# Kernel optimization log

Hardware: AMD Instinct MI355X
Metric: run time of the kernel (lower is better)

Reference implementation:

```python
import jax, jax.numpy as jnp
import numpy as np

B, T, D = 512, 64, 512      # batch, encoder seq len, input_dim
H, A = 256, 256             # hidden_dim, attention_dim (= embed dim)
C = 96                      # num_classes = len(charsets) + 2
STEPS = 26                  # max_len_labels + 1
STD = 0.01


def setup_inputs() -> dict:
    key = jax.random.key(0)
    ks = jax.random.split(key, 14)
    n = lambda k, shape: STD * jax.random.normal(k, shape, jnp.float32)
    return {
        "img": jax.random.normal(ks[0], (B, T, D), jnp.float32),
        "label": jax.random.randint(ks[1], (B, STEPS), 0, C + 1),
        # MLP attention cell
        "Wx": n(ks[2], (A, D)), "bx": jnp.zeros((A,), jnp.float32),
        "Ws": n(ks[3], (A, H)), "bs": jnp.zeros((A,), jnp.float32),
        "Ww": n(ks[4], (1, A)), "bw": jnp.zeros((1,), jnp.float32),
        # target embedding (num_classes + 1 rows)
        "emb": n(ks[5], (C + 1, A)),
        # single-layer GRU, input size D + A, hidden H (torch gate order r,z,n)
        "Wih": n(ks[6], (3 * H, D + A)), "bih": jnp.zeros((3 * H,), jnp.float32),
        "Whh": n(ks[7], (3 * H, H)),     "bhh": jnp.zeros((3 * H,), jnp.float32),
        # output FC
        "Wfc": n(ks[8], (C, H)), "bfc": jnp.zeros((C,), jnp.float32),
    }


def reference(img, label, Wx, bx, Ws, bs, Ww, bw, emb, Wih, Whh, bih, bhh, Wfc, bfc):
    # Precompute xProj once: it is constant across decode steps.
    xProj = jnp.einsum('btd,ad->bta', img, Wx) + bx          # [B,T,A]
    # Teacher forcing: y at step 0 is 0 ([GO]); step i>=1 uses label[:, i].
    y_seq = label.at[:, 0].set(0)                            # [B,STEPS]

    def step(h, y):                                          # h: [B,H], y: [B]
        sProj = h @ Ws.T + bs                                # [B,A]
        e = jnp.tanh(sProj[:, None, :] + xProj)              # [B,T,A]
        v = jnp.einsum('bta,a->bt', e, Ww[0]) + bw[0]        # [B,T]
        alpha = jax.nn.softmax(v, axis=1)
        ctx = jnp.einsum('bt,btd->bd', alpha, img)           # [B,D]
        g = jnp.concatenate([emb[y], ctx], axis=1)           # [B,A+D]
        gi = g @ Wih.T + bih                                 # [B,3H]
        gh = h @ Whh.T + bhh                                 # [B,3H]
        r = jax.nn.sigmoid(gi[:, :H] + gh[:, :H])
        z = jax.nn.sigmoid(gi[:, H:2 * H] + gh[:, H:2 * H])
        nn_ = jnp.tanh(gi[:, 2 * H:] + r * gh[:, 2 * H:])
        h_new = (1.0 - z) * nn_ + z * h
        out = h_new @ Wfc.T + bfc                            # [B,C]
        return h_new, out

    h0 = jnp.zeros((img.shape[0], H), img.dtype)
    _, outs = jax.lax.scan(step, h0, y_seq.T)                # [STEPS,B,C]
    return jnp.transpose(outs, (1, 0, 2))                    # [B,STEPS,C]
```

## Files before the change

kernel.cpp:

```cpp
#include <hip/hip_runtime.h>
#include <math.h>

#define NB 512
#define NT 64
#define ND 512
#define NH 256
#define NA 256
#define NC 96
#define NSTEPS 26
#define NGRU 1152
#define KGRU 768

typedef __attribute__((ext_vector_type(8))) short short8;
typedef __attribute__((ext_vector_type(4))) float f32x4;

static __device__ __forceinline__ unsigned short f2bf(float f) {
    unsigned int u = __float_as_uint(f);
    unsigned int r = (u + 0x7FFFu + ((u >> 16) & 1u)) >> 16;
    return (unsigned short)r;
}
static __device__ __forceinline__ float bf2f(unsigned short u) {
    return __uint_as_float(((unsigned int)u) << 16);
}

__global__ __launch_bounds__(256) void k_prep(
    const float* __restrict__ Wx, const float* __restrict__ Ws,
    const float* __restrict__ Wfc, const float* __restrict__ Wih,
    const float* __restrict__ Whh,
    unsigned short* __restrict__ Wxbf, unsigned short* __restrict__ Wsbf,
    unsigned short* __restrict__ WfcT, unsigned short* __restrict__ Wp)
{
    const int idx = blockIdx.x * 256 + threadIdx.x;
    if (idx < NGRU * KGRU) {
        const int n = idx / KGRU, k = idx - n * KGRU;
        float val = 0.f;
        if (n < 1024) {
            const int j = n >> 2, g = n & 3;
            if (k < 512) {
                if (g == 0)      val = Wih[j * 768 + 256 + k];
                else if (g == 1) val = Wih[(256 + j) * 768 + 256 + k];
                else if (g == 2) val = Wih[(512 + j) * 768 + 256 + k];
            } else {
                const int kh = k - 512;
                if (g == 0)      val = Whh[j * 256 + kh];
                else if (g == 1) val = Whh[(256 + j) * 256 + kh];
                else if (g == 3) val = Whh[(512 + j) * 256 + kh];
            }
        } else if (n < 1120) {
            if (k >= 512) val = Wfc[(n - 1024) * 256 + (k - 512)];
        }
        Wp[idx] = f2bf(val);
    }
    if (idx < 131072) Wxbf[idx] = f2bf(Wx[idx]);
    if (idx < 65536)  Wsbf[idx] = f2bf(Ws[idx]);
    if (idx < 24576) {
        const int k = idx / 96, c = idx % 96;
        WfcT[idx] = f2bf(Wfc[c * 256 + k]);
    }
}

__global__ __launch_bounds__(256) void k_prep2(
    const float* __restrict__ emb, const float* __restrict__ Wih,
    const float* __restrict__ bih, const float* __restrict__ bhh,
    const float* __restrict__ bfc, float* __restrict__ P)
{
    const int y = blockIdx.x;
    const int n = blockIdx.y * 256 + threadIdx.x;
    __shared__ float embS[256];
    embS[threadIdx.x] = emb[y * 256 + threadIdx.x];
    __syncthreads();
    if (n >= NGRU) return;

    float bias = 0.f;
    const float* src = nullptr;
    if (n < 1024) {
        const int j = n >> 2, g = n & 3;
        if (g == 0)      { bias = bih[j] + bhh[j];             src = Wih + (size_t)j * 768; }
        else if (g == 1) { bias = bih[256 + j] + bhh[256 + j]; src = Wih + (size_t)(256 + j) * 768; }
        else if (g == 2) { bias = bih[512 + j];                src = Wih + (size_t)(512 + j) * 768; }
        else             { bias = bhh[512 + j]; }
    } else if (n < 1120) {
        bias = bfc[n - 1024];
    }
    float sp = bias;
    if (src) {
#pragma unroll 8
        for (int k = 0; k < 256; ++k) sp = fmaf(embS[k], src[k], sp);
    }
    P[(size_t)y * NGRU + n] = sp;
}

__global__ __launch_bounds__(256) void k_convert(
    const float* __restrict__ img, unsigned short* __restrict__ imgbf)
{
    const int idx = (blockIdx.x * 256 + threadIdx.x) * 8;
    const float4 v0 = *(const float4*)(img + idx);
    const float4 v1 = *(const float4*)(img + idx + 4);
    short8 o;
    o[0] = (short)f2bf(v0.x); o[1] = (short)f2bf(v0.y);
    o[2] = (short)f2bf(v0.z); o[3] = (short)f2bf(v0.w);
    o[4] = (short)f2bf(v1.x); o[5] = (short)f2bf(v1.y);
    o[6] = (short)f2bf(v1.z); o[7] = (short)f2bf(v1.w);
    *(short8*)(imgbf + idx) = o;
}

__global__ __launch_bounds__(256) void k_xproj(
    const float* __restrict__ img, const unsigned short* __restrict__ imgbf,
    int use_bf, const unsigned short* __restrict__ Wxbf,
    const float* __restrict__ bx, unsigned short* __restrict__ xProjbf)
{
    __shared__ unsigned short As[64][40];
    __shared__ unsigned short Bs[64][40];

    const int tid = threadIdx.x;
    const int lane = tid & 63;
    const int w = tid >> 6;
    const int l15 = lane & 15;
    const int q = lane >> 4;
    const int bm = blockIdx.x * 64;
    const int bn = blockIdx.y * 64;
    const int srow = tid >> 2;
    const int sc0 = (tid & 3) * 8;

    f32x4 acc[4];
#pragma unroll
    for (int i = 0; i < 4; ++i) acc[i] = (f32x4){0.f, 0.f, 0.f, 0.f};

    for (int k0 = 0; k0 < ND; k0 += 32) {
        if (use_bf) {
            *(short8*)&As[srow][sc0] =
                *(const short8*)(imgbf + (size_t)(bm + srow) * ND + k0 + sc0);
        } else {
            const float* ap = img + (size_t)(bm + srow) * ND + k0 + sc0;
            const float4 v0 = *(const float4*)ap;
            const float4 v1 = *(const float4*)(ap + 4);
            short8 av;
            av[0] = (short)f2bf(v0.x); av[1] = (short)f2bf(v0.y);
            av[2] = (short)f2bf(v0.z); av[3] = (short)f2bf(v0.w);
            av[4] = (short)f2bf(v1.x); av[5] = (short)f2bf(v1.y);
            av[6] = (short)f2bf(v1.z); av[7] = (short)f2bf(v1.w);
            *(short8*)&As[srow][sc0] = av;
        }
        *(short8*)&Bs[srow][sc0] =
            *(const short8*)(Wxbf + (size_t)(bn + srow) * ND + k0 + sc0);
        __syncthreads();

        const short8 bf = *(const short8*)&Bs[w * 16 + l15][q * 8];
#pragma unroll
        for (int mt = 0; mt < 4; ++mt) {
            const short8 af = *(const short8*)&As[mt * 16 + l15][q * 8];
            acc[mt] = __builtin_amdgcn_mfma_f32_16x16x32_bf16(af, bf, acc[mt], 0, 0, 0);
        }
        __syncthreads();
    }

#pragma unroll
    for (int mt = 0; mt < 4; ++mt) {
        const int col = bn + w * 16 + l15;
        const float bxv = bx[col];
#pragma unroll
        for (int r = 0; r < 4; ++r) {
            const int row = bm + mt * 16 + q * 4 + r;
            xProjbf[(size_t)row * NA + col] = f2bf(acc[mt][r] + bxv);
        }
    }
}

__global__ __launch_bounds__(256) void k_gru(
    const unsigned short* __restrict__ Ain, unsigned short* __restrict__ Aout,
    const unsigned short* __restrict__ Wp, const float* __restrict__ P,
    const int* __restrict__ label, float* __restrict__ h,
    float* __restrict__ out, int s)
{
    __shared__ unsigned short As[32][40];
    __shared__ unsigned short Bs[64][40];
    __shared__ float CS[32][65];
    __shared__ int yS[32];

    const int tid = threadIdx.x;
    const int lane = tid & 63;
    const int w = tid >> 6;
    const int l15 = lane & 15;
    const int q = lane >> 4;
    const int bm = blockIdx.x * 32;
    const int bn = blockIdx.y * 64;
    const int srow = tid >> 2;
    const int sc0 = (tid & 3) * 8;

    if (tid < 32)
        yS[tid] = (s == 0) ? 0 : label[(bm + tid) * NSTEPS + s];

    f32x4 acc[2];
    acc[0] = (f32x4){0.f, 0.f, 0.f, 0.f};
    acc[1] = (f32x4){0.f, 0.f, 0.f, 0.f};

    for (int k0 = 0; k0 < KGRU; k0 += 32) {
        *(short8*)&Bs[srow][sc0] =
            *(const short8*)(Wp + (size_t)(bn + srow) * KGRU + k0 + sc0);
        if (tid < 128)
            *(short8*)&As[srow][sc0] =
                *(const short8*)(Ain + (size_t)(bm + srow) * KGRU + k0 + sc0);
        __syncthreads();

        const short8 bf = *(const short8*)&Bs[w * 16 + l15][q * 8];
#pragma unroll
        for (int mt = 0; mt < 2; ++mt) {
            const short8 af = *(const short8*)&As[mt * 16 + l15][q * 8];
            acc[mt] = __builtin_amdgcn_mfma_f32_16x16x32_bf16(af, bf, acc[mt], 0, 0, 0);
        }
        __syncthreads();
    }

    const int col = bn + w * 16 + l15;
    if (blockIdx.y < 16) {
#pragma unroll
        for (int mt = 0; mt < 2; ++mt)
#pragma unroll
            for (int r = 0; r < 4; ++r) {
                const int row = mt * 16 + q * 4 + r;
                CS[row][w * 16 + l15] = acc[mt][r] + P[(size_t)yS[row] * NGRU + col];
            }
        __syncthreads();
#pragma unroll
        for (int it = 0; it < 2; ++it) {
            const int u = tid + 256 * it;
            const int row = u >> 4;
            const int jl = u & 15;
            const float r_pre = CS[row][4 * jl + 0];
            const float z_pre = CS[row][4 * jl + 1];
            const float ni    = CS[row][4 * jl + 2];
            const float nh    = CS[row][4 * jl + 3];
            const float r = 1.f / (1.f + expf(-r_pre));
            const float z = 1.f / (1.f + expf(-z_pre));
            const float n = tanhf(fmaf(r, nh, ni));
            const int b = bm + row;
            const int j = (bn >> 2) + jl;
            const float hp = h[b * NH + j];
            const float hn = (1.f - z) * n + z * hp;
            h[b * NH + j] = hn;
            Aout[(size_t)b * KGRU + 512 + j] = f2bf(hn);
        }
    } else {
        if (s >= 1) {
            const int c = col - 1024;
            if (c < NC) {
#pragma unroll
                for (int mt = 0; mt < 2; ++mt)
#pragma unroll
                    for (int r = 0; r < 4; ++r) {
                        const int row = mt * 16 + q * 4 + r;
                        out[((size_t)(bm + row) * NSTEPS + (s - 1)) * NC + c] =
                            acc[mt][r] + P[(size_t)yS[row] * NGRU + col];
                    }
            }
        }
    }
}

__global__ __launch_bounds__(256) void k_sproj(
    const unsigned short* __restrict__ Ahs, const unsigned short* __restrict__ Wsbf,
    const float* __restrict__ bs, float* __restrict__ sProj, int init)
{
    const int tid = threadIdx.x;
    const int b0 = blockIdx.x * 64;
    const int n0 = blockIdx.y * 64;

    if (init) {
        const int c = tid & 63, rg = tid >> 6;
        const float bv = bs[n0 + c];
#pragma unroll
        for (int i = 0; i < 16; ++i)
            sProj[(size_t)(b0 + rg * 16 + i) * NA + n0 + c] = bv;
        return;
    }

    __shared__ unsigned short As[64][72];
    __shared__ unsigned short Bs[64][72];

    const int lane = tid & 63;
    const int w = tid >> 6;
    const int l15 = lane & 15;
    const int q = lane >> 4;

    f32x4 acc[4];
#pragma unroll
    for (int i = 0; i < 4; ++i) acc[i] = (f32x4){0.f, 0.f, 0.f, 0.f};

    for (int k0 = 0; k0 < NH; k0 += 64) {
#pragma unroll
        for (int rep = 0; rep < 2; ++rep) {
            const int ch = tid + rep * 256;
            const int row = ch >> 3, col8 = (ch & 7) * 8;
            *(short8*)&As[row][col8] =
                *(const short8*)(Ahs + (size_t)(b0 + row) * KGRU + 512 + k0 + col8);
            *(short8*)&Bs[row][col8] =
                *(const short8*)(Wsbf + (size_t)(n0 + row) * NH + k0 + col8);
        }
        __syncthreads();
#pragma unroll
        for (int kk = 0; kk < 64; kk += 32) {
            const short8 bf = *(const short8*)&Bs[w * 16 + l15][kk + q * 8];
#pragma unroll
            for (int mt = 0; mt < 4; ++mt) {
                const short8 af = *(const short8*)&As[mt * 16 + l15][kk + q * 8];
                acc[mt] = __builtin_amdgcn_mfma_f32_16x16x32_bf16(af, bf, acc[mt], 0, 0, 0);
            }
        }
        __syncthreads();
    }

    const int col = n0 + w * 16 + l15;
    const float bv = bs[col];
#pragma unroll
    for (int mt = 0; mt < 4; ++mt)
#pragma unroll
        for (int r = 0; r < 4; ++r)
            sProj[(size_t)(b0 + mt * 16 + q * 4 + r) * NA + col] = acc[mt][r] + bv;
}

__global__ __launch_bounds__(512) void k_att(
    float* __restrict__ h, unsigned short* __restrict__ Aout,
    const float* __restrict__ sProj,
    const unsigned short* __restrict__ imgbf, const float* __restrict__ imgf,
    int use_bf, const unsigned short* __restrict__ xProjbf,
    const float* __restrict__ Ww, const float* __restrict__ bw, int step)
{
    const int b = blockIdx.x;
    const int tid = threadIdx.x;
    const int lane = tid & 63;
    const int w = tid >> 6;

    __shared__ float sS[NA];
    __shared__ float wwS[NA];
    __shared__ float vS[NT];
    __shared__ float alphaS[NT];
    __shared__ float ctxS[8][512];

    if (tid < 256) {
        sS[tid] = sProj[b * NA + tid];
        wwS[tid] = Ww[tid];
        if (step < 0) {
            h[b * NH + tid] = 0.f;
            Aout[(size_t)b * KGRU + 512 + tid] = 0;
        }
    }
    __syncthreads();

    const int a0 = (lane & 31) * 8;
    float ss[8], ww[8];
#pragma unroll
    for (int i = 0; i < 8; ++i) {
        ss[i] = sS[a0 + i];
        ww[i] = wwS[a0 + i];
    }
    const float bw0 = bw[0];
#pragma unroll 2
    for (int p = 0; p < 4; ++p) {
        const int t = w * 8 + p * 2 + (lane >> 5);
        const short8 x8 = *(const short8*)(xProjbf + ((size_t)(b * NT + t)) * NA + a0);
        float s = 0.f;
#pragma unroll
        for (int i = 0; i < 8; ++i)
            s += ww[i] * tanhf(ss[i] + bf2f((unsigned short)x8[i]));
#pragma unroll
        for (int off = 16; off > 0; off >>= 1) s += __shfl_xor(s, off);
        if ((lane & 31) == 0) vS[t] = s + bw0;
    }
    __syncthreads();

    if (w == 0) {
        float v = vS[lane];
        float m = v;
#pragma unroll
        for (int off = 32; off > 0; off >>= 1) m = fmaxf(m, __shfl_xor(m, off));
        float e = expf(v - m);
        float ssum = e;
#pragma unroll
        for (int off = 32; off > 0; off >>= 1) ssum += __shfl_xor(ssum, off);
        alphaS[lane] = e / ssum;
    }
    __syncthreads();

    const int d0 = lane * 8;
    float c[8];
#pragma unroll
    for (int i = 0; i < 8; ++i) c[i] = 0.f;

    if (use_bf) {
        const unsigned short* ib = imgbf + (size_t)b * NT * ND + d0;
#pragma unroll 2
        for (int i = 0; i < 8; ++i) {
            const int t = w + 8 * i;
            const float al = alphaS[t];
            const short8 v = *(const short8*)(ib + (size_t)t * ND);
#pragma unroll
            for (int k = 0; k < 8; ++k)
                c[k] = fmaf(al, bf2f((unsigned short)v[k]), c[k]);
        }
    } else {
        const float* ib = imgf + (size_t)b * NT * ND + d0;
#pragma unroll 2
        for (int i = 0; i < 8; ++i) {
            const int t = w + 8 * i;
            const float al = alphaS[t];
            const float4 v0 = *(const float4*)(ib + (size_t)t * ND);
            const float4 v1 = *(const float4*)(ib + (size_t)t * ND + 4);
            c[0] = fmaf(al, v0.x, c[0]); c[1] = fmaf(al, v0.y, c[1]);
            c[2] = fmaf(al, v0.z, c[2]); c[3] = fmaf(al, v0.w, c[3]);
            c[4] = fmaf(al, v1.x, c[4]); c[5] = fmaf(al, v1.y, c[5]);
            c[6] = fmaf(al, v1.z, c[6]); c[7] = fmaf(al, v1.w, c[7]);
        }
    }
    *(f32x4*)&ctxS[w][d0] = (f32x4){c[0], c[1], c[2], c[3]};
    *(f32x4*)&ctxS[w][d0 + 4] = (f32x4){c[4], c[5], c[6], c[7]};
    __syncthreads();

    float cx = ctxS[0][tid] + ctxS[1][tid] + ctxS[2][tid] + ctxS[3][tid]
             + ctxS[4][tid] + ctxS[5][tid] + ctxS[6][tid] + ctxS[7][tid];
    Aout[(size_t)b * KGRU + tid] = f2bf(cx);
}

__global__ __launch_bounds__(128) void k_fc(
    const float* __restrict__ h, const unsigned short* __restrict__ WfcT,
    const float* __restrict__ bfc, float* __restrict__ out)
{
    const int b = blockIdx.x;
    const int j = threadIdx.x;
    __shared__ float hS[NH];
    hS[j] = h[b * NH + j];
    hS[128 + j] = h[b * NH + 128 + j];
    __syncthreads();
    if (j < NC) {
        float acc = bfc[j];
#pragma unroll 8
        for (int k = 0; k < NH; ++k)
            acc = fmaf(hS[k], bf2f(WfcT[k * NC + j]), acc);
        out[((size_t)b * NSTEPS + (NSTEPS - 1)) * NC + j] = acc;
    }
}

extern "C" void kernel_launch(void* const* d_in, const int* in_sizes, int n_in,
                              void* d_out, int out_size, void* d_ws, size_t ws_size,
                              hipStream_t stream)
{
    const float* img   = (const float*)d_in[0];
    const int*   label = (const int*)d_in[1];
    const float* Wx    = (const float*)d_in[2];
    const float* bx    = (const float*)d_in[3];
    const float* Ws    = (const float*)d_in[4];
    const float* bs    = (const float*)d_in[5];
    const float* Ww    = (const float*)d_in[6];
    const float* bw    = (const float*)d_in[7];
    const float* emb   = (const float*)d_in[8];
    const float* Wih   = (const float*)d_in[9];
    const float* bih   = (const float*)d_in[10];
    const float* Whh   = (const float*)d_in[11];
    const float* bhh   = (const float*)d_in[12];
    const float* Wfc   = (const float*)d_in[13];
    const float* bfc   = (const float*)d_in[14];
    float* out = (float*)d_out;

    float* ws = (float*)d_ws;
    float* h     = ws;
    float* sProj = h + 131072;
    float* P     = sProj + 131072;
    unsigned short* xProjbf = (unsigned short*)(P + 111744);
    unsigned short* A0   = xProjbf + 8388608;
    unsigned short* A1   = A0 + 393216;
    unsigned short* Wp   = A1 + 393216;
    unsigned short* Wxbf = Wp + 884736;
    unsigned short* Wsbf = Wxbf + 131072;
    unsigned short* WfcT = Wsbf + 65536;
    unsigned short* imgbf = WfcT + 24576;

    const size_t need_bf = (size_t)((char*)(imgbf + 16777216) - (char*)d_ws);
    const int use_bf = (ws_size >= need_bf) ? 1 : 0;

    k_prep<<<dim3(3456), dim3(256), 0, stream>>>(
        Wx, Ws, Wfc, Wih, Whh, Wxbf, Wsbf, WfcT, Wp);

    k_prep2<<<dim3(97, 5), dim3(256), 0, stream>>>(
        emb, Wih, bih, bhh, bfc, P);

    if (use_bf)
        k_convert<<<dim3(8192), dim3(256), 0, stream>>>(img, imgbf);

    k_xproj<<<dim3((NB * NT) / 64, NA / 64), dim3(256), 0, stream>>>(
        img, imgbf, use_bf, Wxbf, bx, xProjbf);

    k_sproj<<<dim3(8, 4), dim3(256), 0, stream>>>(A0, Wsbf, bs, sProj, 1);
    k_att<<<dim3(NB), dim3(512), 0, stream>>>(
        h, A0, sProj, imgbf, img, use_bf, xProjbf, Ww, bw, -1);

    for (int s = 0; s < NSTEPS; ++s) {
        unsigned short* Ain  = (s & 1) ? A1 : A0;
        unsigned short* Aout = (s & 1) ? A0 : A1;

        k_gru<<<dim3(16, 18), dim3(256), 0, stream>>>(
            Ain, Aout, Wp, P, label, h, out, s);

        if (s < NSTEPS - 1) {
            k_sproj<<<dim3(8, 4), dim3(256), 0, stream>>>(Aout, Wsbf, bs, sProj, 0);
            k_att<<<dim3(NB), dim3(512), 0, stream>>>(
                h, Aout, sProj, imgbf, img, use_bf, xProjbf, Ww, bw, s);
        }
    }

    k_fc<<<dim3(NB), dim3(128), 0, stream>>>(h, WfcT, bfc, out);
}
```

Before: 982.6 us.

## Retile GRU GEMM to 16-row blocks with full A-row staging in LDS

The per-step GRU kernel now uses 16-row by 64-column tiles with 128 threads, doubling the grid to 32x18 blocks. The whole 16x768 A slice is loaded into shared memory once up front, and the K loop steps by 64 so it needs half as many barrier pairs, with each wave computing two N subtiles. The intent is more blocks in flight, which matters for this latency-bound small GEMM, plus fewer synchronizations. The cost is that Wp is streamed by twice as many blocks and each block uses more LDS.

After: 836.6 us. -14.9%, faster.

```diff
diff --git a/kernel.cpp b/kernel.cpp
--- a/kernel.cpp
+++ b/kernel.cpp
@@ -166,64 +166,78 @@
     }
 }
 
-__global__ __launch_bounds__(256) void k_gru(
+__global__ __launch_bounds__(128) void k_gru(
     const unsigned short* __restrict__ Ain, unsigned short* __restrict__ Aout,
     const unsigned short* __restrict__ Wp, const float* __restrict__ P,
     const int* __restrict__ label, float* __restrict__ h,
     float* __restrict__ out, int s)
 {
-    __shared__ unsigned short As[32][40];
-    __shared__ unsigned short Bs[64][40];
-    __shared__ float CS[32][65];
-    __shared__ int yS[32];
+    __shared__ unsigned short Af[16][776];
+    __shared__ unsigned short Bs[64][72];
+    __shared__ float CS[16][65];
+    __shared__ int yS[16];
 
     const int tid = threadIdx.x;
     const int lane = tid & 63;
     const int w = tid >> 6;
     const int l15 = lane & 15;
     const int q = lane >> 4;
-    const int bm = blockIdx.x * 32;
+    const int bm = blockIdx.x * 16;
     const int bn = blockIdx.y * 64;
-    const int srow = tid >> 2;
-    const int sc0 = (tid & 3) * 8;
-
-    if (tid < 32)
-        yS[tid] = (s == 0) ? 0 : label[(bm + tid) * NSTEPS + s];
+
+    if (tid < 16) yS[tid] = (s == 0) ? 0 : label[(bm + tid) * NSTEPS + s];
+
+#pragma unroll
+    for (int i = 0; i < 12; ++i) {
+        const int c = tid + 128 * i;
+        const int row = c / 96;
+        const int col8 = (c - row * 96) * 8;
+        *(short8*)&Af[row][col8] =
+            *(const short8*)(Ain + (size_t)(bm + row) * KGRU + col8);
+    }
 
     f32x4 acc[2];
     acc[0] = (f32x4){0.f, 0.f, 0.f, 0.f};
     acc[1] = (f32x4){0.f, 0.f, 0.f, 0.f};
 
-    for (int k0 = 0; k0 < KGRU; k0 += 32) {
-        *(short8*)&Bs[srow][sc0] =
-            *(const short8*)(Wp + (size_t)(bn + srow) * KGRU + k0 + sc0);
-        if (tid < 128)
-            *(short8*)&As[srow][sc0] =
-                *(const short8*)(Ain + (size_t)(bm + srow) * KGRU + k0 + sc0);
-        __syncthreads();
-
-        const short8 bf = *(const short8*)&Bs[w * 16 + l15][q * 8];
-#pragma unroll
-        for (int mt = 0; mt < 2; ++mt) {
-            const short8 af = *(const short8*)&As[mt * 16 + l15][q * 8];
-            acc[mt] = __builtin_amdgcn_mfma_f32_16x16x32_bf16(af, bf, acc[mt], 0, 0, 0);
-        }
-        __syncthreads();
-    }
-
-    const int col = bn + w * 16 + l15;
+    for (int k0 = 0; k0 < KGRU; k0 += 64) {
+#pragma unroll
+        for (int i = 0; i < 4; ++i) {
+            const int c = tid + 128 * i;
+            const int row = c >> 3, col8 = (c & 7) * 8;
+            *(short8*)&Bs[row][col8] =
+                *(const short8*)(Wp + (size_t)(bn + row) * KGRU + k0 + col8);
+        }
+        __syncthreads();
+#pragma unroll
+        for (int kk = 0; kk < 64; kk += 32) {
+            const short8 af = *(const short8*)&Af[l15][k0 + kk + q * 8];
+#pragma unroll
+            for (int nt = 0; nt < 2; ++nt) {
+                const short8 bf = *(const short8*)&Bs[(w * 2 + nt) * 16 + l15][kk + q * 8];
+                acc[nt] = __builtin_amdgcn_mfma_f32_16x16x32_bf16(af, bf, acc[nt], 0, 0, 0);
+            }
+        }
+        __syncthreads();
+    }
+
     if (blockIdx.y < 16) {
 #pragma unroll
-        for (int mt = 0; mt < 2; ++mt)
-#pragma unroll
-            for (int r = 0; r < 4; ++r) {
-                const int row = mt * 16 + q * 4 + r;
-                CS[row][w * 16 + l15] = acc[mt][r] + P[(size_t)yS[row] * NGRU + col];
-            }
+        for (int nt = 0; nt < 2; ++nt) {
+            const int cl = (w * 2 + nt) * 16 + l15;
+            const float pv0 = P[(size_t)yS[q * 4 + 0] * NGRU + bn + cl];
+            const float pv1 = P[(size_t)yS[q * 4 + 1] * NGRU + bn + cl];
+            const float pv2 = P[(size_t)yS[q * 4 + 2] * NGRU + bn + cl];
+            const float pv3 = P[(size_t)yS[q * 4 + 3] * NGRU + bn + cl];
+            CS[q * 4 + 0][cl] = acc[nt][0] + pv0;
+            CS[q * 4 + 1][cl] = acc[nt][1] + pv1;
+            CS[q * 4 + 2][cl] = acc[nt][2] + pv2;
+            CS[q * 4 + 3][cl] = acc[nt][3] + pv3;
+        }
         __syncthreads();
 #pragma unroll
         for (int it = 0; it < 2; ++it) {
-            const int u = tid + 256 * it;
+            const int u = tid + 128 * it;
             const int row = u >> 4;
             const int jl = u & 15;
             const float r_pre = CS[row][4 * jl + 0];
@@ -242,16 +256,18 @@
         }
     } else {
         if (s >= 1) {
-            const int c = col - 1024;
-            if (c < NC) {
-#pragma unroll
-                for (int mt = 0; mt < 2; ++mt)
+#pragma unroll
+            for (int nt = 0; nt < 2; ++nt) {
+                const int col = bn + (w * 2 + nt) * 16 + l15;
+                const int c = col - 1024;
+                if (c < NC) {
 #pragma unroll
                     for (int r = 0; r < 4; ++r) {
-                        const int row = mt * 16 + q * 4 + r;
+                        const int row = q * 4 + r;
                         out[((size_t)(bm + row) * NSTEPS + (s - 1)) * NC + c] =
-                            acc[mt][r] + P[(size_t)yS[row] * NGRU + col];
+                            acc[nt][r] + P[(size_t)yS[row] * NGRU + col];
                     }
+                }
             }
         }
     }
@@ -496,7 +512,7 @@
         unsigned short* Ain  = (s & 1) ? A1 : A0;
         unsigned short* Aout = (s & 1) ? A0 : A1;
 
-        k_gru<<<dim3(16, 18), dim3(256), 0, stream>>>(
+        k_gru<<<dim3(32, 18), dim3(128), 0, stream>>>(
             Ain, Aout, Wp, P, label, h, out, s);
 
         if (s < NSTEPS - 1) {
```
